# Optimization experiments

Hardware: AMD Instinct MI355X
Metric: run time of the kernel (lower is better)

Reference implementation:

```python
import jax, jax.numpy as jnp
import numpy as np

B, N, P = 64, 800000, 128          # batch, total CpG features, n_pathways (capsules)
H1, H2, C = 256, 128, 32           # MLP hidden_topology and n_output
EPS = 1e-5                         # BatchNorm1d eps


def _xavier(key, fan_in, fan_out, shape):
    bound = np.sqrt(6.0 / (fan_in + fan_out))
    return jax.random.uniform(key, shape, jnp.float32, -bound, bound)


def setup_inputs() -> dict:
    key = jax.random.key(0)
    ks = jax.random.split(key, 10)
    x = jax.random.normal(ks[0], (B, N), jnp.float32)
    # idx: sorted pathway assignment, equal capsule sizes N//P (matches module_lens)
    idx = jnp.sort(jax.random.randint(ks[1], (N,), 0, P)).astype(jnp.int64)
    # SPWModulesLayer.weight: xavier_uniform on shape (1, N)
    w = _xavier(ks[2], N, 1, (N,))
    co_w = jax.random.uniform(ks[3], (P,), jnp.float32, 0.0, 4.0)  # CancelOut init
    bn0_g, bn0_b = jnp.ones(P, jnp.float32), jnp.zeros(P, jnp.float32)
    W1, b1 = _xavier(ks[4], P, H1, (P, H1)), jnp.zeros(H1, jnp.float32)
    bn1_g, bn1_b = jnp.ones(H1, jnp.float32), jnp.zeros(H1, jnp.float32)
    W2, b2 = _xavier(ks[5], H1, H2, (H1, H2)), jnp.zeros(H2, jnp.float32)
    bn2_g, bn2_b = jnp.ones(H2, jnp.float32), jnp.zeros(H2, jnp.float32)
    Wo, bo = _xavier(ks[6], H2, C, (H2, C)), jnp.zeros(C, jnp.float32)
    return {"x": x, "w": w, "co_w": co_w,
            "bn0_g": bn0_g, "bn0_b": bn0_b,
            "W1": W1, "b1": b1, "bn1_g": bn1_g, "bn1_b": bn1_b,
            "W2": W2, "b2": b2, "bn2_g": bn2_g, "bn2_b": bn2_b,
            "Wo": Wo, "bo": bo, "idx": idx}


def _bn(z, g, b):
    # BatchNorm1d in training mode: batch mean, biased variance
    m = jnp.mean(z, axis=0)
    v = jnp.mean((z - m) ** 2, axis=0)
    return (z - m) * jax.lax.rsqrt(v + EPS) * g + b


def reference(x, w, co_w, bn0_g, bn0_b, W1, b1, bn1_g, bn1_b,
              W2, b2, bn2_g, bn2_b, Wo, bo, idx):
    # --- SPWModulesLayer: weighted scatter_add over pathway index (last dim) ---
    WX = jnp.zeros((x.shape[0], P), x.dtype).at[:, idx].add(x * w)   # [B, P]
    Z = _bn(jax.nn.relu(WX), bn0_g, bn0_b)                           # ReLU + BN
    Z = Z * jax.nn.sigmoid(co_w)                                     # CancelOut
    # --- MLP head: Linear->ReLU->BN twice, then Linear->Softmax ---
    h = _bn(jax.nn.relu(Z @ W1 + b1), bn1_g, bn1_b)
    h = _bn(jax.nn.relu(h @ W2 + b2), bn2_g, bn2_b)
    y = jax.nn.softmax(h @ Wo + bo, axis=-1)
    return (y, Z)
```

## Files before the change

kernel.cpp:

```cpp
#include <hip/hip_runtime.h>
#include <hip/hip_bf16.h>

#define BB     64
#define NF4    200000
#define CHUNKS 3125
#define NP     128
#define NH1    256
#define NH2    128
#define NC     32
#define EPSV   1e-5f

typedef float fx4 __attribute__((ext_vector_type(4)));

#define AS_G __attribute__((address_space(1)))
#define AS_L __attribute__((address_space(3)))

__device__ __forceinline__ float dot4(fx4 a, fx4 b) {
    return fmaf(a[0], b[0], fmaf(a[1], b[1], fmaf(a[2], b[2], a[3] * b[3])));
}

__global__ __launch_bounds__(64) void k_scatter(
    const float* __restrict__ x, const float* __restrict__ w,
    const int* __restrict__ idx, float* __restrict__ WX)
{
    __shared__ char lds[8 * 1024];
    const int lane = threadIdx.x;
    const int wid  = blockIdx.x;
    const int ch   = wid >> 1;
    const int bh   = (wid & 1) << 5;
    const int n4   = ch * 64 + lane;

    const fx4*  __restrict__ w4 = reinterpret_cast<const fx4*>(w);
    const int4* __restrict__ p4 = reinterpret_cast<const int4*>(idx);
    const fx4*  __restrict__ x4 = reinterpret_cast<const fx4*>(x);

    const fx4  wv = w4[n4];
    const int4 pv = p4[n4];
    const int  pLo = __builtin_amdgcn_readfirstlane(pv.x);
    const int  pHi = __shfl(pv.w, 63);
    const bool uniform = (pLo == pHi);

    fx4 wLo, wHi;
    wLo[0] = (pv.x == pLo) ? wv[0] : 0.f;  wHi[0] = (pv.x == pHi) ? wv[0] : 0.f;
    wLo[1] = (pv.y == pLo) ? wv[1] : 0.f;  wHi[1] = (pv.y == pHi) ? wv[1] : 0.f;
    wLo[2] = (pv.z == pLo) ? wv[2] : 0.f;  wHi[2] = (pv.z == pHi) ? wv[2] : 0.f;
    wLo[3] = (pv.w == pLo) ? wv[3] : 0.f;  wHi[3] = (pv.w == pHi) ? wv[3] : 0.f;

    auto stage = [&](int bi) {
        const float* gp = (const float*)(x4 + ((size_t)(bh + bi) * NF4 + n4));
        __builtin_amdgcn_global_load_lds((const AS_G float*)gp,
                                         (AS_L float*)(lds + (bi & 7) * 1024),
                                         16, 0, 0);
    };

    #pragma unroll
    for (int i = 0; i < 7; ++i) stage(i);

    #pragma unroll
    for (int i = 0; i < 32; ++i) {
        if (i < 25) {
            stage(i + 7);
            asm volatile("s_waitcnt vmcnt(6)" ::: "memory");
        } else if (i == 25) {
            asm volatile("s_waitcnt vmcnt(0)" ::: "memory");
        }

        const unsigned laddr =
            (unsigned)(size_t)(AS_L char*)(lds + (i & 7) * 1024 + lane * 16);
        fx4 xr;
        asm volatile("ds_read_b128 %0, %1\n\ts_waitcnt lgkmcnt(0)"
                     : "=v"(xr) : "v"(laddr));

        float sLo = dot4(xr, wLo);
        if (uniform) {
            #pragma unroll
            for (int off = 1; off < 64; off <<= 1)
                sLo += __shfl_xor(sLo, off);
            if (lane == 0)
                atomicAdd(&WX[(bh + i) * NP + pLo], sLo);
        } else {
            float sHi = dot4(xr, wHi);
            #pragma unroll
            for (int off = 1; off < 64; off <<= 1) {
                sLo += __shfl_xor(sLo, off);
                sHi += __shfl_xor(sHi, off);
            }
            if (lane == 0) {
                atomicAdd(&WX[(bh + i) * NP + pLo], sLo);
                atomicAdd(&WX[(bh + i) * NP + pHi], sHi);
            }
        }
    }
}

__global__ void k_zero(float* __restrict__ WX)
{
    const int i = blockIdx.x * 256 + threadIdx.x;
    if (i < BB * NP) WX[i] = 0.f;
}

__device__ __forceinline__ float bn_shfl(float a, float gj, float bj)
{
    float s = a, q = a * a;
    #pragma unroll
    for (int off = 32; off > 0; off >>= 1) {
        s += __shfl_xor(s, off);
        q += __shfl_xor(q, off);
    }
    const float m   = s * (1.f / BB);
    const float var = q * (1.f / BB) - m * m;
    return (a - m) * rsqrtf(var + EPSV) * gj + bj;
}

__global__ __launch_bounds__(256) void k_fc1z(
    const float* __restrict__ WX,   const float* __restrict__ co_w,
    const float* __restrict__ bn0g, const float* __restrict__ bn0b,
    const float* __restrict__ W1,   const float* __restrict__ b1,
    const float* __restrict__ bn1g, const float* __restrict__ bn1b,
    float* __restrict__ Zout, float* __restrict__ h1t)
{
    __shared__ float Zl[NP * 65];
    const int tid  = threadIdx.x;
    const int wv   = tid >> 6;
    const int lane = tid & 63;
    const int blk  = blockIdx.x;

    if (tid < NP) {
        const int p = tid;
        float sum = 0.f, sq = 0.f;
        #pragma unroll 8
        for (int b = 0; b < BB; ++b) {
            const float r = fmaxf(WX[b * NP + p], 0.f);
            sum += r; sq += r * r;
        }
        const float m   = sum * (1.f / BB);
        const float var = sq * (1.f / BB) - m * m;
        const float sc  = rsqrtf(var + EPSV) * bn0g[p];
        const float bt  = bn0b[p];
        const float sig = 1.f / (1.f + expf(-co_w[p]));
        #pragma unroll 8
        for (int b = 0; b < BB; ++b) {
            const float r = fmaxf(WX[b * NP + p], 0.f);
            const float z = ((r - m) * sc + bt) * sig;
            Zl[p * 65 + b] = z;
            if (blk == 0) Zout[b * NP + p] = z;
        }
    }
    __syncthreads();

    const int j = blk * 4 + wv;
    float acc = b1[j];
    #pragma unroll 8
    for (int k = 0; k < NP; ++k)
        acc = fmaf(Zl[k * 65 + lane], W1[k * NH1 + j], acc);
    h1t[j * BB + lane] = bn_shfl(fmaxf(acc, 0.f), bn1g[j], bn1b[j]);
}

template <int K, int NOUT>
__global__ void k_fc_bn_t(const float* __restrict__ in_t,
                          const float* __restrict__ W,
                          const float* __restrict__ bias,
                          const float* __restrict__ g,
                          const float* __restrict__ beta,
                          float* __restrict__ out_t)
{
    const int j = blockIdx.x;
    const int b = threadIdx.x;
    float acc = bias[j];
    #pragma unroll 8
    for (int k = 0; k < K; ++k)
        acc = fmaf(in_t[k * BB + b], W[k * NOUT + j], acc);
    out_t[j * BB + b] = bn_shfl(fmaxf(acc, 0.f), g[j], beta[j]);
}

__global__ void k_head(const float* __restrict__ h2t,
                       const float* __restrict__ Wo,
                       const float* __restrict__ bo,
                       float* __restrict__ y)
{
    const int b = blockIdx.x;
    const int c = threadIdx.x;
    float acc = bo[c];
    #pragma unroll 8
    for (int k = 0; k < NH2; ++k)
        acc = fmaf(h2t[k * BB + b], Wo[k * NC + c], acc);
    float mx = acc;
    #pragma unroll
    for (int off = 16; off > 0; off >>= 1)
        mx = fmaxf(mx, __shfl_xor(mx, off));
    const float e = expf(acc - mx);
    float s = e;
    #pragma unroll
    for (int off = 16; off > 0; off >>= 1)
        s += __shfl_xor(s, off);
    y[b * NC + c] = e / s;
}

extern "C" void kernel_launch(void* const* d_in, const int* in_sizes, int n_in,
                              void* d_out, int out_size, void* d_ws, size_t ws_size,
                              hipStream_t stream)
{
    const float* x    = (const float*)d_in[0];
    const float* w    = (const float*)d_in[1];
    const float* co_w = (const float*)d_in[2];
    const float* bn0g = (const float*)d_in[3];
    const float* bn0b = (const float*)d_in[4];
    const float* W1   = (const float*)d_in[5];
    const float* b1   = (const float*)d_in[6];
    const float* bn1g = (const float*)d_in[7];
    const float* bn1b = (const float*)d_in[8];
    const float* W2   = (const float*)d_in[9];
    const float* b2   = (const float*)d_in[10];
    const float* bn2g = (const float*)d_in[11];
    const float* bn2b = (const float*)d_in[12];
    const float* Wo   = (const float*)d_in[13];
    const float* bo   = (const float*)d_in[14];
    const int*   idx  = (const int*)d_in[15];

    float* out = (float*)d_out;
    float* y   = out;
    float* Z   = out + BB * NC;

    float* WX  = (float*)d_ws;
    float* h1t = WX + BB * NP;
    float* h2t = h1t + BB * NH1;

    k_zero<<<32, 256, 0, stream>>>(WX);
    k_scatter<<<CHUNKS * 2, 64, 0, stream>>>(x, w, idx, WX);
    k_fc1z<<<64, 256, 0, stream>>>(WX, co_w, bn0g, bn0b,
                                   W1, b1, bn1g, bn1b, Z, h1t);
    k_fc_bn_t<NH1, NH2><<<NH2, BB, 0, stream>>>(h1t, W2, b2, bn2g, bn2b, h2t);
    k_head<<<BB, NC, 0, stream>>>(h2t, Wo, bo, y);
}
```

Before: 91.85 us.

## Issue all x loads up front and batch wave reductions via transpose-style shuffle

The scatter kernel now issues all 32 row loads into a 32 KB LDS buffer before waiting, instead of keeping an 8-deep rotating pipeline. After the loads it computes all 32 partial dot products and reduces them together with a butterfly transpose: each shuffle step halves the values each lane holds. This needs about 32 shuffles in total rather than 6 per row, and the final atomics are spread across 32 lanes instead of coming one at a time from lane 0. The cost is higher LDS use per block (32 KB vs 8 KB), which lowers occupancy, and more registers for the accumulator arrays.

```diff
diff --git a/kernel.cpp b/kernel.cpp
--- a/kernel.cpp
+++ b/kernel.cpp
@@ -1,5 +1,6 @@
 #include <hip/hip_runtime.h>
 #include <hip/hip_bf16.h>
+#include <type_traits>
 
 #define BB     64
 #define NF4    200000
@@ -19,11 +20,47 @@
     return fmaf(a[0], b[0], fmaf(a[1], b[1], fmaf(a[2], b[2], a[3] * b[3])));
 }
 
+template <int N, int I = 0, typename F>
+__device__ __forceinline__ void static_for(F&& f) {
+    if constexpr (I < N) {
+        f(std::integral_constant<int, I>{});
+        static_for<N, I + 1>(f);
+    }
+}
+
+__device__ __forceinline__ int bitrev5(int l) {
+    return ((l & 1) << 4) | ((l & 2) << 2) | (l & 4) | ((l & 8) >> 2) | ((l & 16) >> 4);
+}
+
+template <int C, int M>
+__device__ __forceinline__ void red_step(float* v, int lane) {
+    const bool hi = (lane & M) != 0;
+    #pragma unroll
+    for (int j = 0; j < C / 2; ++j) {
+        float mine  = hi ? v[j + C / 2] : v[j];
+        float other = hi ? v[j]         : v[j + C / 2];
+        v[j] = mine + __shfl_xor(other, M);
+    }
+}
+
+__device__ __forceinline__ void reduce_emit(float* acc, int lane, int bh,
+                                            int path, float* __restrict__ WX) {
+    red_step<32, 1>(acc, lane);
+    red_step<16, 2>(acc, lane);
+    red_step<8,  4>(acc, lane);
+    red_step<4,  8>(acc, lane);
+    red_step<2, 16>(acc, lane);
+    float s = acc[0];
+    s += __shfl_xor(s, 32);
+    if (lane < 32)
+        atomicAdd(&WX[(bh + bitrev5(lane)) * NP + path], s);
+}
+
 __global__ __launch_bounds__(64) void k_scatter(
     const float* __restrict__ x, const float* __restrict__ w,
     const int* __restrict__ idx, float* __restrict__ WX)
 {
-    __shared__ char lds[8 * 1024];
+    __shared__ fx4 lds4[32 * 64];
     const int lane = threadIdx.x;
     const int wid  = blockIdx.x;
     const int ch   = wid >> 1;
@@ -46,50 +83,31 @@
     wLo[2] = (pv.z == pLo) ? wv[2] : 0.f;  wHi[2] = (pv.z == pHi) ? wv[2] : 0.f;
     wLo[3] = (pv.w == pLo) ? wv[3] : 0.f;  wHi[3] = (pv.w == pHi) ? wv[3] : 0.f;
 
-    auto stage = [&](int bi) {
-        const float* gp = (const float*)(x4 + ((size_t)(bh + bi) * NF4 + n4));
+    static_for<32>([&](auto I) {
+        constexpr int i = I.value;
+        const float* gp = (const float*)(x4 + ((size_t)(bh + i) * NF4 + n4));
         __builtin_amdgcn_global_load_lds((const AS_G float*)gp,
-                                         (AS_L float*)(lds + (bi & 7) * 1024),
-                                         16, 0, 0);
-    };
-
-    #pragma unroll
-    for (int i = 0; i < 7; ++i) stage(i);
-
-    #pragma unroll
-    for (int i = 0; i < 32; ++i) {
-        if (i < 25) {
-            stage(i + 7);
-            asm volatile("s_waitcnt vmcnt(6)" ::: "memory");
-        } else if (i == 25) {
-            asm volatile("s_waitcnt vmcnt(0)" ::: "memory");
-        }
-
-        const unsigned laddr =
-            (unsigned)(size_t)(AS_L char*)(lds + (i & 7) * 1024 + lane * 16);
-        fx4 xr;
-        asm volatile("ds_read_b128 %0, %1\n\ts_waitcnt lgkmcnt(0)"
-                     : "=v"(xr) : "v"(laddr));
-
-        float sLo = dot4(xr, wLo);
-        if (uniform) {
-            #pragma unroll
-            for (int off = 1; off < 64; off <<= 1)
-                sLo += __shfl_xor(sLo, off);
-            if (lane == 0)
-                atomicAdd(&WX[(bh + i) * NP + pLo], sLo);
-        } else {
-            float sHi = dot4(xr, wHi);
-            #pragma unroll
-            for (int off = 1; off < 64; off <<= 1) {
-                sLo += __shfl_xor(sLo, off);
-                sHi += __shfl_xor(sHi, off);
-            }
-            if (lane == 0) {
-                atomicAdd(&WX[(bh + i) * NP + pLo], sLo);
-                atomicAdd(&WX[(bh + i) * NP + pHi], sHi);
-            }
-        }
+                                         (AS_L float*)(lds4 + i * 64), 16, 0, 0);
+    });
+    asm volatile("s_waitcnt vmcnt(0)" ::: "memory");
+
+    if (uniform) {
+        float acc[32];
+        static_for<32>([&](auto I) {
+            constexpr int i = I.value;
+            acc[i] = dot4(lds4[i * 64 + lane], wLo);
+        });
+        reduce_emit(acc, lane, bh, pLo, WX);
+    } else {
+        float acc[32], accH[32];
+        static_for<32>([&](auto I) {
+            constexpr int i = I.value;
+            const fx4 xr = lds4[i * 64 + lane];
+            acc[i]  = dot4(xr, wLo);
+            accH[i] = dot4(xr, wHi);
+        });
+        reduce_emit(acc,  lane, bh, pLo, WX);
+        reduce_emit(accH, lane, bh, pHi, WX);
     }
 }
 
```

Measured after the change: 87.51 us. 4.7% less time.

## Restructure scatter kernel to 2 batch rows per thread with direct loads

Applied to the files above, without the earlier changes.

The scatter kernel changes from one 64-thread wave streaming 32 batch rows of a 256-feature chunk through an LDS async-load pipeline to 256-thread blocks. In each block every thread loads its x vectors for two batch rows (b and b+32) straight into registers. Weights and indices are now reloaded for each batch pair instead of being reused across 32 rows, which relies on L2 or the last-level cache to absorb the repeats. The aim is much more parallelism and memory-level concurrency without the hand-coded waitcnt pipeline. Block order puts the 32 batch pairs of one segment next to each other to help cache reuse of w and idx.

```diff
diff --git a/kernel.cpp b/kernel.cpp
--- a/kernel.cpp
+++ b/kernel.cpp
@@ -3,7 +3,7 @@
 
 #define BB     64
 #define NF4    200000
-#define CHUNKS 3125
+#define NSEG   782
 #define NP     128
 #define NH1    256
 #define NH2    128
@@ -12,84 +12,73 @@
 
 typedef float fx4 __attribute__((ext_vector_type(4)));
 
-#define AS_G __attribute__((address_space(1)))
-#define AS_L __attribute__((address_space(3)))
-
 __device__ __forceinline__ float dot4(fx4 a, fx4 b) {
     return fmaf(a[0], b[0], fmaf(a[1], b[1], fmaf(a[2], b[2], a[3] * b[3])));
 }
 
-__global__ __launch_bounds__(64) void k_scatter(
+__global__ __launch_bounds__(256) void k_scatter(
     const float* __restrict__ x, const float* __restrict__ w,
     const int* __restrict__ idx, float* __restrict__ WX)
 {
-    __shared__ char lds[8 * 1024];
-    const int lane = threadIdx.x;
-    const int wid  = blockIdx.x;
-    const int ch   = wid >> 1;
-    const int bh   = (wid & 1) << 5;
-    const int n4   = ch * 64 + lane;
-
-    const fx4*  __restrict__ w4 = reinterpret_cast<const fx4*>(w);
-    const int4* __restrict__ p4 = reinterpret_cast<const int4*>(idx);
-    const fx4*  __restrict__ x4 = reinterpret_cast<const fx4*>(x);
-
-    const fx4  wv = w4[n4];
-    const int4 pv = p4[n4];
-    const int  pLo = __builtin_amdgcn_readfirstlane(pv.x);
-    const int  pHi = __shfl(pv.w, 63);
+    const int blk = blockIdx.x;
+    const int b   = blk & 31;
+    const int seg = blk >> 5;
+    const int tid = threadIdx.x;
+    const int n4  = seg * 256 + tid;
+    const int waveBase = seg * 256 + (tid & ~63);
+    if (waveBase + 63 >= NF4) {
+        if (waveBase >= NF4) return;
+    }
+    if (n4 >= NF4) return;
+    const int lane = tid & 63;
+
+    const int  pLo = idx[waveBase * 4];
+    const int  pHi = idx[waveBase * 4 + 255];
     const bool uniform = (pLo == pHi);
 
-    fx4 wLo, wHi;
-    wLo[0] = (pv.x == pLo) ? wv[0] : 0.f;  wHi[0] = (pv.x == pHi) ? wv[0] : 0.f;
-    wLo[1] = (pv.y == pLo) ? wv[1] : 0.f;  wHi[1] = (pv.y == pHi) ? wv[1] : 0.f;
-    wLo[2] = (pv.z == pLo) ? wv[2] : 0.f;  wHi[2] = (pv.z == pHi) ? wv[2] : 0.f;
-    wLo[3] = (pv.w == pLo) ? wv[3] : 0.f;  wHi[3] = (pv.w == pHi) ? wv[3] : 0.f;
-
-    auto stage = [&](int bi) {
-        const float* gp = (const float*)(x4 + ((size_t)(bh + bi) * NF4 + n4));
-        __builtin_amdgcn_global_load_lds((const AS_G float*)gp,
-                                         (AS_L float*)(lds + (bi & 7) * 1024),
-                                         16, 0, 0);
-    };
-
-    #pragma unroll
-    for (int i = 0; i < 7; ++i) stage(i);
-
-    #pragma unroll
-    for (int i = 0; i < 32; ++i) {
-        if (i < 25) {
-            stage(i + 7);
-            asm volatile("s_waitcnt vmcnt(6)" ::: "memory");
-        } else if (i == 25) {
-            asm volatile("s_waitcnt vmcnt(0)" ::: "memory");
+    const fx4  wv = reinterpret_cast<const fx4*>(w)[n4];
+    const int4 pv = reinterpret_cast<const int4*>(idx)[n4];
+    const fx4  xA = reinterpret_cast<const fx4*>(x)[(size_t)b * NF4 + n4];
+    const fx4  xB = reinterpret_cast<const fx4*>(x)[(size_t)(b + 32) * NF4 + n4];
+
+    fx4 wLo;
+    wLo[0] = (pv.x == pLo) ? wv[0] : 0.f;
+    wLo[1] = (pv.y == pLo) ? wv[1] : 0.f;
+    wLo[2] = (pv.z == pLo) ? wv[2] : 0.f;
+    wLo[3] = (pv.w == pLo) ? wv[3] : 0.f;
+
+    float aLo = dot4(xA, wLo);
+    float bLo = dot4(xB, wLo);
+    #pragma unroll
+    for (int off = 1; off < 64; off <<= 1) {
+        aLo += __shfl_xor(aLo, off);
+        bLo += __shfl_xor(bLo, off);
+    }
+
+    if (uniform) {
+        const float val = (lane == 0) ? aLo : bLo;
+        const int   row = (lane == 0) ? b : (b + 32);
+        if (lane < 2)
+            atomicAdd(&WX[row * NP + pLo], val);
+    } else {
+        fx4 wHi;
+        wHi[0] = (pv.x == pHi) ? wv[0] : 0.f;
+        wHi[1] = (pv.y == pHi) ? wv[1] : 0.f;
+        wHi[2] = (pv.z == pHi) ? wv[2] : 0.f;
+        wHi[3] = (pv.w == pHi) ? wv[3] : 0.f;
+        float aHi = dot4(xA, wHi);
+        float bHi = dot4(xB, wHi);
+        #pragma unroll
+        for (int off = 1; off < 64; off <<= 1) {
+            aHi += __shfl_xor(aHi, off);
+            bHi += __shfl_xor(bHi, off);
         }
-
-        const unsigned laddr =
-            (unsigned)(size_t)(AS_L char*)(lds + (i & 7) * 1024 + lane * 16);
-        fx4 xr;
-        asm volatile("ds_read_b128 %0, %1\n\ts_waitcnt lgkmcnt(0)"
-                     : "=v"(xr) : "v"(laddr));
-
-        float sLo = dot4(xr, wLo);
-        if (uniform) {
-            #pragma unroll
-            for (int off = 1; off < 64; off <<= 1)
-                sLo += __shfl_xor(sLo, off);
-            if (lane == 0)
-                atomicAdd(&WX[(bh + i) * NP + pLo], sLo);
-        } else {
-            float sHi = dot4(xr, wHi);
-            #pragma unroll
-            for (int off = 1; off < 64; off <<= 1) {
-                sLo += __shfl_xor(sLo, off);
-                sHi += __shfl_xor(sHi, off);
-            }
-            if (lane == 0) {
-                atomicAdd(&WX[(bh + i) * NP + pLo], sLo);
-                atomicAdd(&WX[(bh + i) * NP + pHi], sHi);
-            }
-        }
+        const float val = (lane == 0) ? aLo : ((lane == 1) ? bLo
+                        : ((lane == 2) ? aHi : bHi));
+        const int   row = ((lane & 1) == 0) ? b : (b + 32);
+        const int   col = (lane < 2) ? pLo : pHi;
+        if (lane < 4)
+            atomicAdd(&WX[row * NP + col], val);
     }
 }
 
@@ -226,7 +215,7 @@
     float* h2t = h1t + BB * NH1;
 
     k_zero<<<32, 256, 0, stream>>>(WX);
-    k_scatter<<<CHUNKS * 2, 64, 0, stream>>>(x, w, idx, WX);
+    k_scatter<<<NSEG * 32, 256, 0, stream>>>(x, w, idx, WX);
     k_fc1z<<<64, 256, 0, stream>>>(WX, co_w, bn0g, bn0b,
                                    W1, b1, bn1g, bn1b, Z, h1t);
     k_fc_bn_t<NH1, NH2><<<NH2, BB, 0, stream>>>(h1t, W2, b2, bn2g, bn2b, h2t);
```

Result: no change. 91.29 us (-0.6%).
